# Performance work log

Hardware: AMD Instinct MI355X
Metric: run time of the kernel (lower is better)

Reference implementation:

```python
import jax, jax.numpy as jnp
import numpy as np

N_HEAD = 4
GROUPS = 32
EPS = 1e-5


def group_norm(x, scale, bias):
    B, C, H, W = x.shape
    xg = x.reshape(B, GROUPS, C // GROUPS, H, W)
    mu = xg.mean(axis=(2, 3, 4), keepdims=True)
    var = xg.var(axis=(2, 3, 4), keepdims=True)
    xg = (xg - mu) * jax.lax.rsqrt(var + EPS)
    x = xg.reshape(B, C, H, W)
    return x * scale[None, :, None, None] + bias[None, :, None, None]


def setup_inputs() -> dict:
    key = jax.random.key(0)
    k0, k1, k2 = jax.random.split(key, 3)
    B, C, H, W = 2, 64, 64, 64
    x = jax.random.normal(k0, (B, C, H, W), dtype=jnp.float32)
    gn_scale = jnp.ones((C,), dtype=jnp.float32)
    gn_bias = jnp.zeros((C,), dtype=jnp.float32)
    w_qkv = jax.random.normal(k1, (3 * C, C), dtype=jnp.float32) * 0.05  # 1x1 conv, no bias
    w_out = jax.random.normal(k2, (C, C), dtype=jnp.float32) * 0.05     # 1x1 conv
    b_out = jnp.zeros((C,), dtype=jnp.float32)
    return {"x": x, "gn_scale": gn_scale, "gn_bias": gn_bias,
            "w_qkv": w_qkv, "w_out": w_out, "b_out": b_out}


def reference(x, gn_scale, gn_bias, w_qkv, w_out, b_out):
    B, C, H, W = x.shape
    head_dim = C // N_HEAD
    norm = group_norm(x, gn_scale, gn_bias)
    # 1x1 conv == channel matmul
    qkv = jnp.einsum('oc,bchw->bohw', w_qkv, norm)
    qkv = qkv.reshape(B, N_HEAD, head_dim * 3, H, W)
    q, k, v = jnp.split(qkv, 3, axis=2)  # each [B, n, head_dim, H, W]
    # full spatial attention scores, scaled by sqrt(channel) as in source
    attn = jnp.einsum('bnchw,bncyx->bnhwyx', q, k) / jnp.sqrt(jnp.float32(C))
    attn = jax.nn.softmax(attn.reshape(B, N_HEAD, H, W, H * W), axis=-1)
    attn = attn.reshape(B, N_HEAD, H, W, H, W)
    out = jnp.einsum('bnhwyx,bncyx->bnchw', attn, v).reshape(B, C, H, W)
    out = jnp.einsum('oc,bchw->bohw', w_out, out) + b_out[None, :, None, None]
    return out + x
```

## Files before the change

kernel.cpp:

```cpp
#include <hip/hip_runtime.h>
#include <hip/hip_bf16.h>

typedef __attribute__((ext_vector_type(8))) short short8;
typedef __attribute__((ext_vector_type(4))) float f32x4;
typedef __attribute__((ext_vector_type(16))) float f32x16;
typedef __attribute__((ext_vector_type(4))) unsigned int uint4v;

#define DEV static __device__ __forceinline__

DEV unsigned short f2bf(float f){
  unsigned u = __float_as_uint(f);
  u += 0x7fffu + ((u >> 16) & 1u);
  return (unsigned short)(u >> 16);
}

DEV unsigned pack2bf(float a, float b){
  __hip_bfloat162 h = __float22bfloat162_rn(make_float2(a, b));
  unsigned u;
  __builtin_memcpy(&u, &h, 4);
  return u;
}

#define QSCALE 0.180336880111f
#define NSPLIT 4
#define NT 16

__global__ __launch_bounds__(256) void gn_partial_k(const float* __restrict__ x,
                                                    float* __restrict__ gp){
  int blk = blockIdx.x;
  float4 v = ((const float4*)(x + (size_t)blk*1024))[threadIdx.x];
  float s = v.x+v.y+v.z+v.w;
  float q = v.x*v.x+v.y*v.y+v.z*v.z+v.w*v.w;
  #pragma unroll
  for (int off = 1; off < 64; off <<= 1){
    s += __shfl_xor(s, off);
    q += __shfl_xor(q, off);
  }
  __shared__ float red[8];
  int w = threadIdx.x >> 6;
  if ((threadIdx.x & 63) == 0){ red[w*2] = s; red[w*2+1] = q; }
  __syncthreads();
  if (threadIdx.x == 0){
    gp[blk*2+0] = red[0]+red[2]+red[4]+red[6];
    gp[blk*2+1] = red[1]+red[3]+red[5]+red[7];
  }
}

__global__ __launch_bounds__(256) void qkv_k(const float* __restrict__ x,
    const float* __restrict__ gp, const float* __restrict__ gsc,
    const float* __restrict__ gbi, const float* __restrict__ wq,
    unsigned short* __restrict__ q, unsigned short* __restrict__ k,
    unsigned short* __restrict__ vt){
  int b  = blockIdx.x >> 8;
  int s0 = (blockIdx.x & 255) * 16;
  __shared__ float W[192][68];
  __shared__ float A[16][68];
  __shared__ float MS[32][2];
  int t = threadIdx.x;
  for (int i = t; i < 3072; i += 256){
    int o = i >> 4, c4 = (i & 15) * 4;
    *(float4*)&W[o][c4] = ((const float4*)wq)[i];
  }
  if (t < 32){
    float s = 0.f, ss = 0.f;
    #pragma unroll
    for (int i = 0; i < 8; ++i){
      const float* pp = gp + ((b*32 + t)*8 + i)*2;
      s += pp[0]; ss += pp[1];
    }
    float mean = s * (1.f/8192.f);
    MS[t][0] = mean;
    MS[t][1] = rsqrtf(ss * (1.f/8192.f) - mean*mean + 1e-5f);
  }
  __syncthreads();
  {
    int c  = t >> 2;
    int s4 = (t & 3) * 4;
    const float* px = x + ((size_t)b*64 + c)*4096 + s0 + s4;
    float4 v0 = *(const float4*)px;
    float sc = gsc[c] * MS[c>>1][1];
    float bi = gbi[c] - MS[c>>1][0] * sc;
    A[s4+0][c]=v0.x*sc+bi; A[s4+1][c]=v0.y*sc+bi;
    A[s4+2][c]=v0.z*sc+bi; A[s4+3][c]=v0.w*sc+bi;
  }
  __syncthreads();
  int sl = t >> 4, grp = t & 15;
  float acc[12];
  #pragma unroll
  for (int j = 0; j < 12; ++j) acc[j] = 0.f;
  for (int c4 = 0; c4 < 16; ++c4){
    float4 a = *(const float4*)&A[sl][c4*4];
    #pragma unroll
    for (int j = 0; j < 12; ++j){
      float4 wv = *(const float4*)&W[grp + j*16][c4*4];
      acc[j] = fmaf(a.x, wv.x, fmaf(a.y, wv.y, fmaf(a.z, wv.z, fmaf(a.w, wv.w, acc[j]))));
    }
  }
  int s = s0 + sl;
  int slp = (sl & 0x3) | (((sl >> 2) & 1) << 3) | (((sl >> 3) & 1) << 2);
  #pragma unroll
  for (int j = 0; j < 12; ++j){
    int o = grp + j*16;
    int n = o / 48, r = o % 48;
    float val = acc[j];
    if (r < 16){
      q[(((size_t)b*4 + n)*4096 + s)*16 + r] = f2bf(val * QSCALE);
    } else if (r < 32){
      k[(((size_t)b*4 + n)*4096 + s)*16 + r - 16] = f2bf(val);
    } else {
      vt[((size_t)(b*4 + n)*16 + (r - 32))*4096 + s0 + slp] = f2bf(val);
    }
  }
}

__global__ __launch_bounds__(512, 4) void attn_k(const unsigned short* __restrict__ qb,
    const unsigned short* __restrict__ kb, const unsigned short* __restrict__ vt,
    float* __restrict__ part, float* __restrict__ lsums){
  int blk = blockIdx.x;
  int bn = blk & 7;
  int sp = (blk >> 3) & (NSPLIT - 1);
  int qg = blk >> 5;
  int t = threadIdx.x, w = t >> 6, l = t & 63;
  int lq = l & 31, hi = l >> 5;

  __shared__ unsigned short Klds[16384];
  __shared__ unsigned short Vlds[16384];

  {
    const unsigned short* ksrc = kb + ((size_t)bn*4096 + sp*1024)*16;
    #pragma unroll
    for (int p = 0; p < 4; ++p){
      int G = p*512 + t;
      *(short8*)&Klds[G*8] = *(const short8*)(ksrc + G*8);
    }
    const unsigned short* vsrc = vt + (size_t)bn*16*4096 + sp*1024;
    #pragma unroll
    for (int p = 0; p < 4; ++p){
      int G = p*512 + t;
      int d = G >> 7, gi = G & 127;
      short8 vv = *(const short8*)(vsrc + (size_t)d*4096 + gi*8);
      *(short8*)&Vlds[d*1024 + ((gi ^ (d & 7)) * 8)] = vv;
    }
  }

  int qrow = qg*256 + w*32;
  short8 qf = *(const short8*)(qb + ((size_t)bn*4096 + qrow)*16 + (size_t)lq*16 + hi*8);

  __syncthreads();

  f32x16 O, zero;
  #pragma unroll
  for (int r = 0; r < 16; ++r){ O[r] = 0.f; zero[r] = 0.f; }

  short8 vsel;
  {
    unsigned short c = (lq == 16) ? (unsigned short)0x3F80 : (unsigned short)0;
    #pragma unroll
    for (int r = 0; r < 8; ++r) vsel[r] = (short)c;
  }

  int vdrow = (lq & 15);
  int vxor  = 8 * (vdrow & 7);
  bool vld = (lq < 16);

  short8 kf0 = *(const short8*)&Klds[(0*64 + 0*32 + lq)*16 + hi*8];
  short8 kf1 = *(const short8*)&Klds[(0*64 + 1*32 + lq)*16 + hi*8];

  #pragma unroll 1
  for (int kt = 0; kt < NT; ++kt){
    short8 v0 = vsel, v1 = vsel, v2 = vsel, v3 = vsel;
    if (vld){
      int base = vdrow*1024 + kt*64 + hi*8;
      v0 = *(const short8*)&Vlds[(base +  0) ^ vxor];
      v1 = *(const short8*)&Vlds[(base + 16) ^ vxor];
      v2 = *(const short8*)&Vlds[(base + 32) ^ vxor];
      v3 = *(const short8*)&Vlds[(base + 48) ^ vxor];
    }
    short8 kn0 = {}, kn1 = {};
    if (kt + 1 < NT){
      kn0 = *(const short8*)&Klds[((kt+1)*64 + lq)*16 + hi*8];
      kn1 = *(const short8*)&Klds[((kt+1)*64 + 32 + lq)*16 + hi*8];
    }

    f32x16 sA = __builtin_amdgcn_mfma_f32_32x32x16_bf16(kf0, qf, zero, 0, 0, 0);
    f32x16 sB = __builtin_amdgcn_mfma_f32_32x32x16_bf16(kf1, qf, zero, 0, 0, 0);

    #pragma unroll
    for (int r = 0; r < 16; ++r) sA[r] = __builtin_amdgcn_exp2f(sA[r]);
    #pragma unroll
    for (int r = 0; r < 16; ++r) sB[r] = __builtin_amdgcn_exp2f(sB[r]);

    auto pvstep = [&](const f32x16& pc, int h8, short8 vf){
      uint4v pw;
      pw[0] = pack2bf(pc[h8+0], pc[h8+1]);
      pw[1] = pack2bf(pc[h8+2], pc[h8+3]);
      pw[2] = pack2bf(pc[h8+4], pc[h8+5]);
      pw[3] = pack2bf(pc[h8+6], pc[h8+7]);
      short8 pa = __builtin_bit_cast(short8, pw);
      O = __builtin_amdgcn_mfma_f32_32x32x16_bf16(pa, vf, O, 0, 0, 0);
    };
    pvstep(sA, 0, v0);
    pvstep(sA, 8, v1);
    pvstep(sB, 0, v2);
    pvstep(sB, 8, v3);

    kf0 = kn0; kf1 = kn1;
  }

  float* Op = part + (((size_t)sp*8 + bn)*4096 + qrow)*16;
  size_t lbase = ((size_t)sp*8 + bn)*4096 + qrow;
  #pragma unroll
  for (int r = 0; r < 16; ++r){
    int qr = (r&3) + 8*(r>>2) + 4*hi;
    if (lq < 16) __builtin_nontemporal_store(O[r], &Op[(size_t)qr*16 + lq]);
  }
  if (lq == 16){
    #pragma unroll
    for (int r = 0; r < 16; ++r){
      int qr = (r&3) + 8*(r>>2) + 4*hi;
      __builtin_nontemporal_store(O[r], &lsums[lbase + qr]);
    }
  }
}

__global__ __launch_bounds__(256) void oproj_k(const float* __restrict__ part,
    const float* __restrict__ lsums, const float* __restrict__ wo,
    const float* __restrict__ bo, const float* __restrict__ x,
    float* __restrict__ out){
  int b  = blockIdx.x >> 8;
  int s0 = (blockIdx.x & 255) * 16;
  __shared__ float W[64][68];
  __shared__ float A[16][68];
  int t = threadIdx.x;
  for (int i = t; i < 1024; i += 256){
    int o = i >> 4, c4 = (i & 15) * 4;
    *(float4*)&W[o][c4] = ((const float4*)wo)[i];
  }
  {
    int sl = t & 15;
    int u  = t >> 4;
    int n = u >> 2, d4 = (u & 3) * 4;
    size_t row = ((size_t)b*4 + n)*4096 + s0 + sl;
    float L = 0.f;
    #pragma unroll
    for (int sp = 0; sp < NSPLIT; ++sp)
      L += __builtin_nontemporal_load(&lsums[(size_t)sp*32768 + row]);
    f32x4 acc = {0.f,0.f,0.f,0.f};
    #pragma unroll
    for (int sp = 0; sp < NSPLIT; ++sp){
      f32x4 u0 = __builtin_nontemporal_load(
          (const f32x4*)(part + ((size_t)sp*32768 + row)*16 + d4));
      acc += u0;
    }
    float inv = 1.f / L;
    A[sl][n*16+d4+0] = acc[0]*inv; A[sl][n*16+d4+1] = acc[1]*inv;
    A[sl][n*16+d4+2] = acc[2]*inv; A[sl][n*16+d4+3] = acc[3]*inv;
  }
  __syncthreads();
  int sl = t & 15, grp = t >> 4;
  float acc[4] = {0.f,0.f,0.f,0.f};
  for (int c4 = 0; c4 < 16; ++c4){
    float4 a = *(const float4*)&A[sl][c4*4];
    #pragma unroll
    for (int j = 0; j < 4; ++j){
      float4 wv = *(const float4*)&W[grp + j*16][c4*4];
      acc[j] = fmaf(a.x, wv.x, fmaf(a.y, wv.y, fmaf(a.z, wv.z, fmaf(a.w, wv.w, acc[j]))));
    }
  }
  int s = s0 + sl;
  #pragma unroll
  for (int j = 0; j < 4; ++j){
    int o = grp + j*16;
    size_t idx = ((size_t)b*64 + o)*4096 + s;
    out[idx] = acc[j] + bo[o] + x[idx];
  }
}

extern "C" void kernel_launch(void* const* d_in, const int* in_sizes, int n_in,
                              void* d_out, int out_size, void* d_ws, size_t ws_size,
                              hipStream_t stream){
  const float* x   = (const float*)d_in[0];
  const float* gsc = (const float*)d_in[1];
  const float* gbi = (const float*)d_in[2];
  const float* wq  = (const float*)d_in[3];
  const float* wo  = (const float*)d_in[4];
  const float* bo  = (const float*)d_in[5];
  float* out = (float*)d_out;

  char* ws = (char*)d_ws;
  float* gp          = (float*)ws;
  unsigned short* q  = (unsigned short*)(ws + 8192);
  unsigned short* k  = (unsigned short*)(ws + 8192 + 1048576);
  unsigned short* vt = (unsigned short*)(ws + 8192 + 2097152);
  float* part        = (float*)(ws + 8192 + 3145728);
  float* lsums       = (float*)(ws + 8192 + 3145728 + 8388608);

  gn_partial_k<<<512, 256, 0, stream>>>(x, gp);
  qkv_k       <<<512, 256, 0, stream>>>(x, gp, gsc, gbi, wq, q, k, vt);
  attn_k      <<<512, 512, 0, stream>>>(q, k, vt, part, lsums);
  oproj_k     <<<512, 256, 0, stream>>>(part, lsums, wo, bo, x, out);
}
```

Before: 57.07 us.

## Split attention into more smaller blocks, read V from global, store partials as bf16

The attention kernel now runs as 2048 blocks of 256 threads, covering 128 queries and 512 keys each, where it was 512 blocks of 512 threads with a 4-way key split. V tiles are no longer staged in LDS. They are loaded directly from global memory, which leaves only K in shared memory and allows more blocks per CU. Partial outputs are stored as bf16 to halve that write/read traffic, and s_setprio wraps the MFMA sections to favour matrix issue. The tradeoffs are more partials to reduce in oproj, uncached global V loads inside the loop, and reduced precision in the partial sums.

```diff
diff --git a/kernel.cpp b/kernel.cpp
--- a/kernel.cpp
+++ b/kernel.cpp
@@ -5,6 +5,7 @@
 typedef __attribute__((ext_vector_type(4))) float f32x4;
 typedef __attribute__((ext_vector_type(16))) float f32x16;
 typedef __attribute__((ext_vector_type(4))) unsigned int uint4v;
+typedef __attribute__((ext_vector_type(4))) unsigned short ushort4v;
 
 #define DEV static __device__ __forceinline__
 
@@ -12,6 +13,13 @@
   unsigned u = __float_as_uint(f);
   u += 0x7fffu + ((u >> 16) & 1u);
   return (unsigned short)(u >> 16);
+}
+
+DEV float bf2f(unsigned short h){
+  unsigned u = ((unsigned)h) << 16;
+  float f;
+  __builtin_memcpy(&f, &u, 4);
+  return f;
 }
 
 DEV unsigned pack2bf(float a, float b){
@@ -22,8 +30,8 @@
 }
 
 #define QSCALE 0.180336880111f
-#define NSPLIT 4
-#define NT 16
+#define NSPLIT 8
+#define NT 8
 
 __global__ __launch_bounds__(256) void gn_partial_k(const float* __restrict__ x,
                                                     float* __restrict__ gp){
@@ -113,44 +121,32 @@
   }
 }
 
-__global__ __launch_bounds__(512, 4) void attn_k(const unsigned short* __restrict__ qb,
+__global__ __launch_bounds__(256, 5) void attn_k(const unsigned short* __restrict__ qb,
     const unsigned short* __restrict__ kb, const unsigned short* __restrict__ vt,
-    float* __restrict__ part, float* __restrict__ lsums){
+    unsigned short* __restrict__ part, float* __restrict__ lsums){
   int blk = blockIdx.x;
   int bn = blk & 7;
   int sp = (blk >> 3) & (NSPLIT - 1);
-  int qg = blk >> 5;
+  int qg = blk >> 6;
   int t = threadIdx.x, w = t >> 6, l = t & 63;
   int lq = l & 31, hi = l >> 5;
 
-  __shared__ unsigned short Klds[16384];
-  __shared__ unsigned short Vlds[16384];
+  __shared__ unsigned short Klds[8192];
 
   {
-    const unsigned short* ksrc = kb + ((size_t)bn*4096 + sp*1024)*16;
+    const unsigned short* ksrc = kb + ((size_t)bn*4096 + sp*512)*16;
     #pragma unroll
     for (int p = 0; p < 4; ++p){
-      int G = p*512 + t;
-      *(short8*)&Klds[G*8] = *(const short8*)(ksrc + G*8);
-    }
-    const unsigned short* vsrc = vt + (size_t)bn*16*4096 + sp*1024;
-    #pragma unroll
-    for (int p = 0; p < 4; ++p){
-      int G = p*512 + t;
-      int d = G >> 7, gi = G & 127;
-      short8 vv = *(const short8*)(vsrc + (size_t)d*4096 + gi*8);
-      *(short8*)&Vlds[d*1024 + ((gi ^ (d & 7)) * 8)] = vv;
-    }
-  }
-
-  int qrow = qg*256 + w*32;
+      int G = p*256 + t;
+      *(short8*)&Klds[G*8] = *(const short8*)(ksrc + (size_t)G*8);
+    }
+  }
+
+  int qrow = qg*128 + w*32;
   short8 qf = *(const short8*)(qb + ((size_t)bn*4096 + qrow)*16 + (size_t)lq*16 + hi*8);
 
-  __syncthreads();
-
-  f32x16 O, zero;
-  #pragma unroll
-  for (int r = 0; r < 16; ++r){ O[r] = 0.f; zero[r] = 0.f; }
+  const unsigned short* vaddr = vt + ((size_t)bn*16 + (lq & 15))*4096 + sp*512 + hi*8;
+  bool vld = (lq < 16);
 
   short8 vsel;
   {
@@ -159,31 +155,35 @@
     for (int r = 0; r < 8; ++r) vsel[r] = (short)c;
   }
 
-  int vdrow = (lq & 15);
-  int vxor  = 8 * (vdrow & 7);
-  bool vld = (lq < 16);
-
-  short8 kf0 = *(const short8*)&Klds[(0*64 + 0*32 + lq)*16 + hi*8];
-  short8 kf1 = *(const short8*)&Klds[(0*64 + 1*32 + lq)*16 + hi*8];
+  f32x16 O, zero;
+  #pragma unroll
+  for (int r = 0; r < 16; ++r){ O[r] = 0.f; zero[r] = 0.f; }
+
+  __syncthreads();
+
+  short8 kf0 = *(const short8*)&Klds[(size_t)lq*16 + hi*8];
+  short8 kf1 = *(const short8*)&Klds[(size_t)(32 + lq)*16 + hi*8];
 
   #pragma unroll 1
   for (int kt = 0; kt < NT; ++kt){
     short8 v0 = vsel, v1 = vsel, v2 = vsel, v3 = vsel;
     if (vld){
-      int base = vdrow*1024 + kt*64 + hi*8;
-      v0 = *(const short8*)&Vlds[(base +  0) ^ vxor];
-      v1 = *(const short8*)&Vlds[(base + 16) ^ vxor];
-      v2 = *(const short8*)&Vlds[(base + 32) ^ vxor];
-      v3 = *(const short8*)&Vlds[(base + 48) ^ vxor];
+      const unsigned short* va = vaddr + (size_t)kt*64;
+      v0 = *(const short8*)(va);
+      v1 = *(const short8*)(va + 16);
+      v2 = *(const short8*)(va + 32);
+      v3 = *(const short8*)(va + 48);
     }
     short8 kn0 = {}, kn1 = {};
     if (kt + 1 < NT){
-      kn0 = *(const short8*)&Klds[((kt+1)*64 + lq)*16 + hi*8];
-      kn1 = *(const short8*)&Klds[((kt+1)*64 + 32 + lq)*16 + hi*8];
-    }
-
+      kn0 = *(const short8*)&Klds[(size_t)((kt+1)*64 + lq)*16 + hi*8];
+      kn1 = *(const short8*)&Klds[(size_t)((kt+1)*64 + 32 + lq)*16 + hi*8];
+    }
+
+    __builtin_amdgcn_s_setprio(1);
     f32x16 sA = __builtin_amdgcn_mfma_f32_32x32x16_bf16(kf0, qf, zero, 0, 0, 0);
     f32x16 sB = __builtin_amdgcn_mfma_f32_32x32x16_bf16(kf1, qf, zero, 0, 0, 0);
+    __builtin_amdgcn_s_setprio(0);
 
     #pragma unroll
     for (int r = 0; r < 16; ++r) sA[r] = __builtin_amdgcn_exp2f(sA[r]);
@@ -199,20 +199,22 @@
       short8 pa = __builtin_bit_cast(short8, pw);
       O = __builtin_amdgcn_mfma_f32_32x32x16_bf16(pa, vf, O, 0, 0, 0);
     };
+    __builtin_amdgcn_s_setprio(1);
     pvstep(sA, 0, v0);
     pvstep(sA, 8, v1);
     pvstep(sB, 0, v2);
     pvstep(sB, 8, v3);
+    __builtin_amdgcn_s_setprio(0);
 
     kf0 = kn0; kf1 = kn1;
   }
 
-  float* Op = part + (((size_t)sp*8 + bn)*4096 + qrow)*16;
+  unsigned short* Op = part + (((size_t)sp*8 + bn)*4096 + qrow)*16;
   size_t lbase = ((size_t)sp*8 + bn)*4096 + qrow;
   #pragma unroll
   for (int r = 0; r < 16; ++r){
     int qr = (r&3) + 8*(r>>2) + 4*hi;
-    if (lq < 16) __builtin_nontemporal_store(O[r], &Op[(size_t)qr*16 + lq]);
+    if (lq < 16) __builtin_nontemporal_store(f2bf(O[r]), &Op[(size_t)qr*16 + lq]);
   }
   if (lq == 16){
     #pragma unroll
@@ -223,7 +225,7 @@
   }
 }
 
-__global__ __launch_bounds__(256) void oproj_k(const float* __restrict__ part,
+__global__ __launch_bounds__(256) void oproj_k(const unsigned short* __restrict__ part,
     const float* __restrict__ lsums, const float* __restrict__ wo,
     const float* __restrict__ bo, const float* __restrict__ x,
     float* __restrict__ out){
@@ -248,9 +250,9 @@
     f32x4 acc = {0.f,0.f,0.f,0.f};
     #pragma unroll
     for (int sp = 0; sp < NSPLIT; ++sp){
-      f32x4 u0 = __builtin_nontemporal_load(
-          (const f32x4*)(part + ((size_t)sp*32768 + row)*16 + d4));
-      acc += u0;
+      ushort4v u0 = *(const ushort4v*)(part + ((size_t)sp*32768 + row)*16 + d4);
+      acc[0] += bf2f(u0[0]); acc[1] += bf2f(u0[1]);
+      acc[2] += bf2f(u0[2]); acc[3] += bf2f(u0[3]);
     }
     float inv = 1.f / L;
     A[sl][n*16+d4+0] = acc[0]*inv; A[sl][n*16+d4+1] = acc[1]*inv;
@@ -288,15 +290,15 @@
   float* out = (float*)d_out;
 
   char* ws = (char*)d_ws;
-  float* gp          = (float*)ws;
-  unsigned short* q  = (unsigned short*)(ws + 8192);
-  unsigned short* k  = (unsigned short*)(ws + 8192 + 1048576);
-  unsigned short* vt = (unsigned short*)(ws + 8192 + 2097152);
-  float* part        = (float*)(ws + 8192 + 3145728);
-  float* lsums       = (float*)(ws + 8192 + 3145728 + 8388608);
-
-  gn_partial_k<<<512, 256, 0, stream>>>(x, gp);
-  qkv_k       <<<512, 256, 0, stream>>>(x, gp, gsc, gbi, wq, q, k, vt);
-  attn_k      <<<512, 512, 0, stream>>>(q, k, vt, part, lsums);
-  oproj_k     <<<512, 256, 0, stream>>>(part, lsums, wo, bo, x, out);
-}
+  float* gp           = (float*)ws;
+  unsigned short* q   = (unsigned short*)(ws + 8192);
+  unsigned short* k   = (unsigned short*)(ws + 8192 + 1048576);
+  unsigned short* vt  = (unsigned short*)(ws + 8192 + 2097152);
+  unsigned short* part= (unsigned short*)(ws + 8192 + 3145728);
+  float* lsums        = (float*)(ws + 8192 + 3145728 + 8388608);
+
+  gn_partial_k<<<512,  256, 0, stream>>>(x, gp);
+  qkv_k       <<<512,  256, 0, stream>>>(x, gp, gsc, gbi, wq, q, k, vt);
+  attn_k      <<<2048, 256, 0, stream>>>(q, k, vt, part, lsums);
+  oproj_k     <<<512,  256, 0, stream>>>(part, lsums, wo, bo, x, out);
+}
```

Result: faster. 55.56 us (-2.7%).
